# Performance work log

Hardware: AMD Instinct MI355X
Metric: run time of the kernel (lower is better)

## Reference

```python
import jax, jax.numpy as jnp
from jax import lax
import numpy as np

B, C, H, W = 16, 256, 96, 96
K = 11            # conv kernel size along one axis
C8 = C // 8       # query/key channels


def _conv(x, w, b):
    # 'same' conv in NCHW with OIHW weights; kernel is (kh,1) or (1,kw)
    kh, kw = w.shape[2], w.shape[3]
    y = lax.conv_general_dilated(
        x, w, window_strides=(1, 1),
        padding=((kh // 2, kh // 2), (kw // 2, kw // 2)),
        dimension_numbers=('NCHW', 'OIHW', 'NCHW'))
    return y + b[None, :, None, None]


def setup_inputs() -> dict:
    key = jax.random.key(0)
    ks = jax.random.split(key, 14)
    s = 0.05
    d = {
        'x':    jax.random.normal(ks[0], (B, C, H, W), jnp.float32),
        'wq_h': jax.random.normal(ks[1], (C8, C, K, 1), jnp.float32) * s,
        'bq_h': jax.random.normal(ks[2], (C8,), jnp.float32) * s,
        'wq_w': jax.random.normal(ks[3], (C8, C, 1, K), jnp.float32) * s,
        'bq_w': jax.random.normal(ks[4], (C8,), jnp.float32) * s,
        'wk_h': jax.random.normal(ks[5], (C8, C, K, 1), jnp.float32) * s,
        'bk_h': jax.random.normal(ks[6], (C8,), jnp.float32) * s,
        'wk_w': jax.random.normal(ks[7], (C8, C, 1, K), jnp.float32) * s,
        'bk_w': jax.random.normal(ks[8], (C8,), jnp.float32) * s,
        'wv_h': jax.random.normal(ks[9], (C, C, K, 1), jnp.float32) * s,
        'bv_h': jax.random.normal(ks[10], (C,), jnp.float32) * s,
        'wv_w': jax.random.normal(ks[11], (C, C, 1, K), jnp.float32) * s,
        'bv_w': jax.random.normal(ks[12], (C,), jnp.float32) * s,
        # gamma is a learned scalar (zero-init in torch); nonzero here so the
        # attention path contributes to the output
        'gamma': jax.random.normal(ks[13], (1,), jnp.float32) * 0.5,
    }
    return d


def reference(x, wq_h, bq_h, wq_w, bq_w, wk_h, bk_h, wk_w, bk_w,
              wv_h, bv_h, wv_w, bv_w, gamma):
    b, c, h, w = x.shape
    q_h = _conv(x, wq_h, bq_h)   # [B, C8, H, W]
    q_w = _conv(x, wq_w, bq_w)
    k_h = _conv(x, wk_h, bk_h)
    k_w = _conv(x, wk_w, bk_w)
    v_h = _conv(x, wv_h, bv_h)   # [B, C, H, W]
    v_w = _conv(x, wv_w, bv_w)
    # column (H-axis) attention energies: [B, H, W, H'] with -inf on h==h'
    e_h = jnp.einsum('bchw,bcHw->bhwH', q_h, k_h)
    diag = jnp.eye(h, dtype=bool)[None, :, None, :]  # [1, H, 1, H']
    e_h = jnp.where(diag, -jnp.inf, e_h)
    # row (W-axis) attention energies: [B, H, W, W']
    e_w = jnp.einsum('bchw,bchW->bhwW', q_w, k_w)
    # joint softmax over concatenated H'+W' axis
    att = jax.nn.softmax(jnp.concatenate([e_h, e_w], axis=-1), axis=-1)
    a_h = att[..., :h]           # [B, H, W, H']
    a_w = att[..., h:]           # [B, H, W, W']
    out_h = jnp.einsum('bcHw,bhwH->bchw', v_h, a_h)
    out_w = jnp.einsum('bchW,bhwW->bchw', v_w, a_w)
    return gamma * (out_h + out_w) + x
```

## Files before the change

kernel.cpp:

```cpp
#include <hip/hip_runtime.h>

constexpr int Bn = 16, Cn = 256, Hn = 96, Wn = 96, Pn = Hn * Wn;

#define DI static __device__ __forceinline__

struct alignas(16) U4 { unsigned a, b, c, d; };

typedef _Float16 f16x8 __attribute__((ext_vector_type(8)));
typedef float f32x4 __attribute__((ext_vector_type(4)));

#define GLOAD16(g, l) __builtin_amdgcn_global_load_lds( \
    (const __attribute__((address_space(1))) void*)(g), \
    (__attribute__((address_space(3))) void*)(l), 16, 0, 0)

__global__ void k_wt16(const float* __restrict__ w, _Float16* __restrict__ wt,
                       int co_n, int co_off, int co_tot) {
    int idx = blockIdx.x * 256 + threadIdx.x;
    if (idx >= co_n * 2816) return;
    int co = idx / 2816;
    int r  = idx - co * 2816;
    int c  = r / 11, t = r - c * 11;
    wt[((size_t)t * co_tot + co_off + co) * 256 + c] = (_Float16)w[idx];
}

__global__ __launch_bounds__(256) void k_xsplit(const float* __restrict__ x,
                                                _Float16* __restrict__ xh, _Float16* __restrict__ xl,
                                                _Float16* __restrict__ xhT, _Float16* __restrict__ xlT) {
    int b = blockIdx.y;
    int tid = threadIdx.x;
    int p = blockIdx.x * 128 + (tid >> 1);
    int half = tid & 1;
    int h = p / 96, w = p - h * 96;
    int pT = w * 96 + h;
    const float* xb = x + (size_t)b * Cn * Pn + p;
    size_t ob  = ((size_t)b * Pn + p) * 256;
    size_t obT = ((size_t)b * Pn + pT) * 256;
    for (int it = 0; it < 16; ++it) {
        int c0 = it * 16 + half * 8;
        f16x8 vh_, vl_;
#pragma unroll
        for (int i = 0; i < 8; ++i) {
            float f = xb[(size_t)(c0 + i) * Pn];
            _Float16 hh = (_Float16)f;
            vh_[i] = hh;
            vl_[i] = (_Float16)(f - (float)hh);
        }
        *(f16x8*)(xh + ob + c0) = vh_;
        *(f16x8*)(xl + ob + c0) = vl_;
        *(f16x8*)(xhT + obT + c0) = vh_;
        *(f16x8*)(xlT + obT + c0) = vl_;
    }
}

__global__ __launch_bounds__(256, 3) void k_conv_v(const _Float16* __restrict__ X0,
                                                   const _Float16* __restrict__ W0,
                                                   const float* __restrict__ b0a,
                                                   _Float16* __restrict__ o0,
                                                   const _Float16* __restrict__ X1,
                                                   const _Float16* __restrict__ W1,
                                                   const float* __restrict__ b1a,
                                                   _Float16* __restrict__ o1) {
    __shared__ char sm_raw[28672];
    const int tid = threadIdx.x;
    const int lane = tid & 63, wave = tid >> 6;
    const int wm = wave >> 1, wn = wave & 1;
    const int l15 = lane & 15, kg = lane >> 4;
    const int bx = blockIdx.x, co0 = blockIdx.y * 64;
    const int fam = blockIdx.z >> 4, b = blockIdx.z & 15;
    const _Float16* X  = fam ? X1 : X0;
    const _Float16* WT = fam ? W1 : W0;
    const float* bias  = fam ? b1a : b0a;
    _Float16* out      = fam ? o1 : o0;

    for (int z = tid; z < 1024; z += 256) {
        int bufo = (z >> 9) * 14336;
        int s = (z >> 7) & 3, off = z & 127;
        int Rbase = (s >> 1) * 112 + ((s & 1) ? 104 : 0);
        *(unsigned*)(sm_raw + bufo + Rbase * 64 + off * 4) = 0u;
    }

    f32x4 acc[2][6];
#pragma unroll
    for (int mf = 0; mf < 2; ++mf) {
        const float* bp = bias + co0 + wm * 32 + mf * 16 + kg * 4;
        f32x4 bv = { bp[0], bp[1], bp[2], bp[3] };
#pragma unroll
        for (int nf = 0; nf < 6; ++nf) acc[mf][nf] = bv;
    }

    const _Float16* Xb = X + ((size_t)b * Pn + bx * 192) * 256;
    const _Float16* Wb = WT + (size_t)(co0 + wm * 32 + l15) * 256 + kg * 8;

    auto STAGE = [&](int c0, int bufo) {
        for (int i = wave; i < 12; i += 4) {
            int rr = i / 6, wch = i - rr * 6;
            int row_local = 8 + wch * 16 + (lane >> 2);
            int kchunk = (lane & 3) ^ ((row_local >> 1) & 3);
            const _Float16* src = Xb + ((size_t)(rr * 96 + row_local - 8)) * 256 + c0 + kchunk * 8;
            char* dst = sm_raw + bufo + (rr * 112 + 8 + wch * 16) * 64;
            GLOAD16(src, dst);
        }
    };
    auto LDA = [&](f16x8* slot, const _Float16* tp) {
#pragma unroll
        for (int mf = 0; mf < 2; ++mf) slot[mf] = *(const f16x8*)(tp + mf * 4096);
    };
    auto LDB = [&](f16x8* dst, const char* Bb, int T) {
        int rl0 = 3 + l15 + T;
        const char* bp = Bb + (wn * 112 + rl0) * 64 + ((kg ^ ((rl0 >> 1) & 3)) << 4);
#pragma unroll
        for (int nf = 0; nf < 6; ++nf) dst[nf] = *(const f16x8*)(bp + nf * 1024);
    };

    STAGE(0, 0);
    __syncthreads();

    int cur = 0;
    for (int s8 = 0; s8 < 8; ++s8) {
        const int c0 = s8 * 32;
        const _Float16* wc = Wb + c0;
        f16x8 afc[2], afn[2];
        LDA(afc, wc);
        if (s8 < 7) STAGE(c0 + 32, (cur ^ 1) * 14336);
        const char* Bb = sm_raw + cur * 14336;
        f16x8 b0f[6], b1f[6];
        LDB(b0f, Bb, 0);
#pragma unroll
        for (int t = 0; t < 11; ++t) {
            if (t < 10) {
                LDA(afn, wc + (t + 1) * 65536);
                LDB((t & 1) ? b0f : b1f, Bb, t + 1);
            }
            const f16x8* bf = (t & 1) ? b1f : b0f;
            __builtin_amdgcn_s_setprio(1);
#pragma unroll
            for (int mf = 0; mf < 2; ++mf)
#pragma unroll
                for (int nf = 0; nf < 6; ++nf)
                    acc[mf][nf] = __builtin_amdgcn_mfma_f32_16x16x32_f16(afc[mf], bf[nf], acc[mf][nf], 0, 0, 0);
            __builtin_amdgcn_s_setprio(0);
            if (t < 10) {
#pragma unroll
                for (int mf = 0; mf < 2; ++mf) afc[mf] = afn[mf];
            }
        }
        __syncthreads();
        cur ^= 1;
    }

    _Float16* sb = (_Float16*)sm_raw;
#pragma unroll
    for (int mf = 0; mf < 2; ++mf)
#pragma unroll
        for (int nf = 0; nf < 6; ++nf)
#pragma unroll
            for (int r = 0; r < 4; ++r) {
                int row = wm * 32 + mf * 16 + kg * 4 + r;
                int p = wn * 96 + nf * 16 + l15;
                sb[row * 192 + p] = (_Float16)acc[mf][nf][r];
            }
    __syncthreads();
    for (int k = 0; k < 6; ++k) {
        int ci = tid + k * 256;
        int row = ci / 24, ch = ci - row * 24;
        U4 v = *(const U4*)(sm_raw + row * 384 + ch * 16);
        *(U4*)(out + ((size_t)b * 256 + co0 + row) * Pn + bx * 192 + ch * 8) = v;
    }
}

__global__ __launch_bounds__(256, 2) void k_conv_qk(const _Float16* __restrict__ Xh0,
                                                    const _Float16* __restrict__ Xl0,
                                                    const _Float16* __restrict__ W0,
                                                    const float* __restrict__ bq0, const float* __restrict__ bk0,
                                                    _Float16* __restrict__ q0, _Float16* __restrict__ k0,
                                                    const _Float16* __restrict__ Xh1,
                                                    const _Float16* __restrict__ Xl1,
                                                    const _Float16* __restrict__ W1,
                                                    const float* __restrict__ bq1, const float* __restrict__ bk1,
                                                    _Float16* __restrict__ q1, _Float16* __restrict__ k1) {
    __shared__ char sm_raw[57344];
    const int tid = threadIdx.x;
    const int lane = tid & 63, wave = tid >> 6;
    const int wm = wave >> 1, wn = wave & 1;
    const int l15 = lane & 15, kg = lane >> 4;
    const int bx = blockIdx.x;
    const int fam = blockIdx.z >> 4, b = blockIdx.z & 15;
    const _Float16* Xh = fam ? Xh1 : Xh0;
    const _Float16* Xl = fam ? Xl1 : Xl0;
    const _Float16* WT = fam ? W1 : W0;
    const float* bq = fam ? bq1 : bq0;
    const float* bk = fam ? bk1 : bk0;
    _Float16* q16 = fam ? q1 : q0;
    _Float16* k16 = fam ? k1 : k0;

    for (int z = tid; z < 2048; z += 256) {
        int bufo = (z >> 10) * 28672;
        int s = (z >> 7) & 7, off = z & 127;
        int Rbase = (s >> 1) * 112 + ((s & 1) ? 104 : 0);
        *(unsigned*)(sm_raw + bufo + Rbase * 64 + off * 4) = 0u;
    }

    f32x4 acc[2][6];
#pragma unroll
    for (int mf = 0; mf < 2; ++mf) {
        int cb = wm * 32 + mf * 16 + kg * 4;
        f32x4 bv;
#pragma unroll
        for (int r = 0; r < 4; ++r) {
            int co_l = cb + r;
            bv[r] = (co_l < 32) ? bq[co_l] : bk[co_l - 32];
        }
#pragma unroll
        for (int nf = 0; nf < 6; ++nf) acc[mf][nf] = bv;
    }

    const _Float16* Xbh = Xh + ((size_t)b * Pn + bx * 192) * 256;
    const _Float16* Xbl = Xl + ((size_t)b * Pn + bx * 192) * 256;
    const _Float16* Wb = WT + (size_t)(wm * 32 + l15) * 256 + kg * 8;

    auto STAGE = [&](int c0, int bufo) {
        for (int i = wave; i < 24; i += 4) {
            int a = i / 12, rr = (i / 6) & 1, wch = i % 6;
            int row_local = 8 + wch * 16 + (lane >> 2);
            int kchunk = (lane & 3) ^ ((row_local >> 1) & 3);
            const _Float16* base = (a == 0) ? Xbh : Xbl;
            const _Float16* src = base + ((size_t)(rr * 96 + row_local - 8)) * 256 + c0 + kchunk * 8;
            char* dst = sm_raw + bufo + ((a * 2 + rr) * 112 + 8 + wch * 16) * 64;
            GLOAD16(src, dst);
        }
    };
    auto LDBHL = [&](f16x8* dh, f16x8* dl, const char* Bb, int T) {
        int rl0 = 3 + l15 + T;
        const char* bp = Bb + (wn * 112 + rl0) * 64 + ((kg ^ ((rl0 >> 1) & 3)) << 4);
#pragma unroll
        for (int nf = 0; nf < 6; ++nf) {
            dh[nf] = *(const f16x8*)(bp + nf * 1024);
            dl[nf] = *(const f16x8*)(bp + 14336 + nf * 1024);
        }
    };

    STAGE(0, 0);
    __syncthreads();

    int cur = 0;
    for (int s8 = 0; s8 < 8; ++s8) {
        const int c0 = s8 * 32;
        const _Float16* wc = Wb + c0;
        f16x8 afc[2], afn[2];
#pragma unroll
        for (int mf = 0; mf < 2; ++mf) afc[mf] = *(const f16x8*)(wc + mf * 4096);
        if (s8 < 7) STAGE(c0 + 32, (cur ^ 1) * 28672);
        const char* Bb = sm_raw + cur * 28672;
#pragma unroll
        for (int t = 0; t < 11; ++t) {
            if (t < 10) {
#pragma unroll
                for (int mf = 0; mf < 2; ++mf)
                    afn[mf] = *(const f16x8*)(wc + (t + 1) * 16384 + mf * 4096);
            }
            f16x8 bh[6], bl[6];
            LDBHL(bh, bl, Bb, t);
            __builtin_amdgcn_s_setprio(1);
#pragma unroll
            for (int mf = 0; mf < 2; ++mf)
#pragma unroll
                for (int nf = 0; nf < 6; ++nf) {
                    acc[mf][nf] = __builtin_amdgcn_mfma_f32_16x16x32_f16(afc[mf], bh[nf], acc[mf][nf], 0, 0, 0);
                    acc[mf][nf] = __builtin_amdgcn_mfma_f32_16x16x32_f16(afc[mf], bl[nf], acc[mf][nf], 0, 0, 0);
                }
            __builtin_amdgcn_s_setprio(0);
            if (t < 10) {
#pragma unroll
                for (int mf = 0; mf < 2; ++mf) afc[mf] = afn[mf];
            }
        }
        __syncthreads();
        cur ^= 1;
    }

    __syncthreads();
    _Float16* sq = (_Float16*)sm_raw;
    _Float16* sk = (_Float16*)(sm_raw + 12288);
#pragma unroll
    for (int mf = 0; mf < 2; ++mf) {
        int cb = wm * 32 + mf * 16 + kg * 4;
#pragma unroll
        for (int r = 0; r < 4; ++r) {
            int co_l = cb + r;
            _Float16* arr = (co_l < 32) ? sq : sk;
            int c = co_l & 31;
#pragma unroll
            for (int nf = 0; nf < 6; ++nf) {
                int p = wn * 96 + nf * 16 + l15;
                arr[p * 32 + c] = (_Float16)acc[mf][nf][r];
            }
        }
    }
    __syncthreads();
    for (int j = 0; j < 6; ++j) {
        int idx = tid + j * 256;
        int mtx = idx >= 768;
        int e = idx - mtx * 768;
        int p = e >> 2, cg2 = e & 3;
        U4 v = *(const U4*)(sm_raw + mtx * 12288 + p * 64 + cg2 * 16);
        _Float16* dstb = mtx ? k16 : q16;
        *(U4*)(dstb + ((size_t)b * Pn + bx * 192 + p) * 32 + cg2 * 8) = v;
    }
}

DI void stage_qk16(const _Float16* qg, const _Float16* kg, char* Lq, char* Lk, int tid) {
    for (int i = tid; i < 768; i += 256) {
        int mtx = i >= 384;
        int e = i - mtx * 384;
        int p = e >> 2, ch = e & 3;
        const _Float16* src = (mtx ? kg : qg) + p * 32 + ch * 8;
        f16x8 v = *(const f16x8*)src;
        char* dst = (mtx ? Lk : Lq) + p * 64 + ((ch ^ ((p >> 1) & 3)) << 4);
        *(f16x8*)dst = v;
    }
}

DI void mfma_e(const char* Lq, const char* Lk, float* Ef, int lane, int wave) {
    int l15 = lane & 15, kg = lane >> 4;
    int wm = wave >> 1, wn = wave & 1;
    f16x8 qa[3], kb[3];
#pragma unroll
    for (int i = 0; i < 3; ++i) {
        int pr = wm * 48 + i * 16 + l15;
        qa[i] = *(const f16x8*)(Lq + pr * 64 + ((kg ^ ((pr >> 1) & 3)) << 4));
        int pc = wn * 48 + i * 16 + l15;
        kb[i] = *(const f16x8*)(Lk + pc * 64 + ((kg ^ ((pc >> 1) & 3)) << 4));
    }
#pragma unroll
    for (int i = 0; i < 3; ++i)
#pragma unroll
        for (int j = 0; j < 3; ++j) {
            f32x4 a = { 0.f, 0.f, 0.f, 0.f };
            a = __builtin_amdgcn_mfma_f32_16x16x32_f16(qa[i], kb[j], a, 0, 0, 0);
#pragma unroll
            for (int r = 0; r < 4; ++r) {
                int row = wm * 48 + i * 16 + kg * 4 + r;
                int col = wn * 48 + j * 16 + l15;
                Ef[row * 97 + col] = a[r];
            }
        }
}

__global__ __launch_bounds__(256) void k_p1(const _Float16* __restrict__ q16, const _Float16* __restrict__ k16,
                                            float* __restrict__ mh, float* __restrict__ lh) {
    __shared__ char L[49536];
    float* Ef = (float*)L;
    char* Lq = L + 37248;
    char* Lk = L + 43392;
    const int tid = threadIdx.x, lane = tid & 63, wave = tid >> 6;
    const int w = blockIdx.x, b = blockIdx.y;
    const _Float16* qg = q16 + ((size_t)b * Pn + w * 96) * 32;
    const _Float16* kg = k16 + ((size_t)b * Pn + w * 96) * 32;
    stage_qk16(qg, kg, Lq, Lk, tid);
    __syncthreads();
    mfma_e(Lq, Lk, Ef, lane, wave);
    __syncthreads();
    if (tid < 96) {
        int h = tid;
        const float* er = Ef + h * 97;
        float m = -INFINITY;
        for (int j = 0; j < 96; ++j) if (j != h) m = fmaxf(m, er[j]);
        float l = 0.f;
        for (int j = 0; j < 96; ++j) if (j != h) l += __expf(er[j] - m);
        mh[((size_t)b * 96 + w) * 96 + h] = m;
        lh[((size_t)b * 96 + w) * 96 + h] = l;
    }
}

__global__ __launch_bounds__(256) void k_p2(const _Float16* __restrict__ q16, const _Float16* __restrict__ k16,
                                            const _Float16* __restrict__ V,
                                            const float* __restrict__ mh, const float* __restrict__ lh,
                                            float* __restrict__ mo, float* __restrict__ lo,
                                            _Float16* __restrict__ outw) {
    __shared__ char L[56448];
    float* Ef = (float*)L;
    char* LA  = L + 37248;
    char* Lq  = L + 37248;
    char* Lk  = L + 43392;
    float* Marr = (float*)(L + 55680);
    float* Linv = (float*)(L + 56064);
    const int tid = threadIdx.x, lane = tid & 63, wave = tid >> 6;
    const int l15 = lane & 15, kg = lane >> 4;
    const int h = blockIdx.x, b = blockIdx.y;
    const _Float16* qg = q16 + ((size_t)b * Pn + h * 96) * 32;
    const _Float16* kgp = k16 + ((size_t)b * Pn + h * 96) * 32;
    stage_qk16(qg, kgp, Lq, Lk, tid);
    __syncthreads();
    mfma_e(Lq, Lk, Ef, lane, wave);
    __syncthreads();
    if (tid < 96) {
        int wq = tid;
        const float* er = Ef + wq * 97;
        float mw = -INFINITY;
        for (int j = 0; j < 96; ++j) mw = fmaxf(mw, er[j]);
        float lw = 0.f;
        for (int j = 0; j < 96; ++j) lw += __expf(er[j] - mw);
        float mhv = mh[((size_t)b * 96 + wq) * 96 + h];
        float lhv = lh[((size_t)b * 96 + wq) * 96 + h];
        float m = fmaxf(mhv, mw);
        float l = lhv * __expf(mhv - m) + lw * __expf(mw - m);
        mo[((size_t)b * 96 + h) * 96 + wq] = m;
        lo[((size_t)b * 96 + h) * 96 + wq] = l;
        Marr[wq] = m;
        Linv[wq] = 1.f / l;
    }
    __syncthreads();
    if (tid < 192) {
        int r = tid >> 1, half = tid & 1;
        float m = Marr[r], li = Linv[r];
        const float* er = Ef + r * 97;
        for (int cc = 0; cc < 6; ++cc) {
            int chunk = half * 6 + cc;
            f16x8 av;
#pragma unroll
            for (int jj = 0; jj < 8; ++jj)
                av[jj] = (_Float16)(__expf(er[chunk * 8 + jj] - m) * li);
            *(f16x8*)(LA + r * 192 + ((chunk ^ ((r >> 1) & 3)) << 4)) = av;
        }
    }
    __syncthreads();
    f32x4 acc[4][6];
#pragma unroll
    for (int mf = 0; mf < 4; ++mf)
#pragma unroll
        for (int nf = 0; nf < 6; ++nf) acc[mf][nf] = f32x4{ 0.f, 0.f, 0.f, 0.f };
    const _Float16* vb = V + ((size_t)b * 256 + wave * 64 + l15) * Pn + h * 96 + kg * 8;
    f16x8 va[4][3];
#pragma unroll
    for (int mf = 0; mf < 4; ++mf)
#pragma unroll
        for (int ks = 0; ks < 3; ++ks)
            va[mf][ks] = *(const f16x8*)(vb + (size_t)mf * 16 * Pn + ks * 32);
#pragma unroll
    for (int ks = 0; ks < 3; ++ks)
#pragma unroll
        for (int nf = 0; nf < 6; ++nf) {
            int wq = nf * 16 + l15;
            int chunk = ks * 4 + kg;
            f16x8 bv = *(const f16x8*)(LA + wq * 192 + ((chunk ^ ((wq >> 1) & 3)) << 4));
#pragma unroll
            for (int mf = 0; mf < 4; ++mf)
                acc[mf][nf] = __builtin_amdgcn_mfma_f32_16x16x32_f16(va[mf][ks], bv, acc[mf][nf], 0, 0, 0);
        }
    _Float16* ob = outw + ((size_t)b * 256) * Pn + h * 96;
#pragma unroll
    for (int mf = 0; mf < 4; ++mf)
#pragma unroll
        for (int nf = 0; nf < 6; ++nf)
#pragma unroll
            for (int r = 0; r < 4; ++r) {
                int c = wave * 64 + mf * 16 + kg * 4 + r;
                ob[(size_t)c * Pn + nf * 16 + l15] = (_Float16)acc[mf][nf][r];
            }
}

__global__ __launch_bounds__(256) void k_p3(const _Float16* __restrict__ q16, const _Float16* __restrict__ k16,
                                            const _Float16* __restrict__ V,
                                            const float* __restrict__ mo, const float* __restrict__ lo,
                                            _Float16* __restrict__ pT) {
    __shared__ char L[56448];
    float* Ef = (float*)L;
    char* LA  = L + 37248;
    char* Lq  = L + 37248;
    char* Lk  = L + 43392;
    float* Marr = (float*)(L + 55680);
    float* Linv = (float*)(L + 56064);
    const int tid = threadIdx.x, lane = tid & 63, wave = tid >> 6;
    const int l15 = lane & 15, kg = lane >> 4;
    const int w = blockIdx.x, b = blockIdx.y;
    const _Float16* qg = q16 + ((size_t)b * Pn + w * 96) * 32;
    const _Float16* kgp = k16 + ((size_t)b * Pn + w * 96) * 32;
    stage_qk16(qg, kgp, Lq, Lk, tid);
    __syncthreads();
    mfma_e(Lq, Lk, Ef, lane, wave);
    __syncthreads();
    if (tid < 96) {
        int hq = tid;
        Marr[hq] = mo[((size_t)b * 96 + hq) * 96 + w];
        Linv[hq] = 1.f / lo[((size_t)b * 96 + hq) * 96 + w];
    }
    __syncthreads();
    if (tid < 192) {
        int r = tid >> 1, half = tid & 1;
        float m = Marr[r], li = Linv[r];
        const float* er = Ef + r * 97;
        for (int cc = 0; cc < 6; ++cc) {
            int chunk = half * 6 + cc;
            f16x8 av;
#pragma unroll
            for (int jj = 0; jj < 8; ++jj) {
                int col = chunk * 8 + jj;
                av[jj] = (col == r) ? (_Float16)0.f
                                    : (_Float16)(__expf(er[col] - m) * li);
            }
            *(f16x8*)(LA + r * 192 + ((chunk ^ ((r >> 1) & 3)) << 4)) = av;
        }
    }
    __syncthreads();
    f32x4 acc[4][6];
#pragma unroll
    for (int mf = 0; mf < 4; ++mf)
#pragma unroll
        for (int nf = 0; nf < 6; ++nf) acc[mf][nf] = f32x4{ 0.f, 0.f, 0.f, 0.f };
    const _Float16* vb = V + ((size_t)b * 256 + wave * 64 + l15) * Pn + w * 96 + kg * 8;
    f16x8 va[4][3];
#pragma unroll
    for (int mf = 0; mf < 4; ++mf)
#pragma unroll
        for (int ks = 0; ks < 3; ++ks)
            va[mf][ks] = *(const f16x8*)(vb + (size_t)mf * 16 * Pn + ks * 32);
#pragma unroll
    for (int ks = 0; ks < 3; ++ks)
#pragma unroll
        for (int nf = 0; nf < 6; ++nf) {
            int hq = nf * 16 + l15;
            int chunk = ks * 4 + kg;
            f16x8 bv = *(const f16x8*)(LA + hq * 192 + ((chunk ^ ((hq >> 1) & 3)) << 4));
#pragma unroll
            for (int mf = 0; mf < 4; ++mf)
                acc[mf][nf] = __builtin_amdgcn_mfma_f32_16x16x32_f16(va[mf][ks], bv, acc[mf][nf], 0, 0, 0);
        }
    _Float16* pb = pT + ((size_t)b * 256) * Pn + w * 96;
#pragma unroll
    for (int mf = 0; mf < 4; ++mf)
#pragma unroll
        for (int nf = 0; nf < 6; ++nf)
#pragma unroll
            for (int r = 0; r < 4; ++r) {
                int c = wave * 64 + mf * 16 + kg * 4 + r;
                pb[(size_t)c * Pn + nf * 16 + l15] = (_Float16)acc[mf][nf][r];
            }
}

__global__ __launch_bounds__(256) void k_combine(const _Float16* __restrict__ pT,
                                                 const _Float16* __restrict__ ow,
                                                 const float* __restrict__ x,
                                                 const float* __restrict__ gamma,
                                                 float* __restrict__ out) {
    __shared__ float T[32][33];
    int bh = blockIdx.x, bw = blockIdx.y;
    size_t ib = (size_t)blockIdx.z * Pn;
    int tx = threadIdx.x, ty = threadIdx.y;
#pragma unroll
    for (int i = 0; i < 4; ++i) {
        int r = bw * 32 + ty + i * 8;
        T[ty + i * 8][tx] = (float)pT[ib + (size_t)r * 96 + bh * 32 + tx];
    }
    __syncthreads();
    float g = gamma[0];
#pragma unroll
    for (int i = 0; i < 4; ++i) {
        int hh = bh * 32 + ty + i * 8, ww = bw * 32 + tx;
        size_t o = ib + (size_t)hh * 96 + ww;
        out[o] = g * (T[tx][ty + i * 8] + (float)ow[o]) + x[o];
    }
}

extern "C" void kernel_launch(void* const* d_in, const int* in_sizes, int n_in,
                              void* d_out, int out_size, void* d_ws, size_t ws_size,
                              hipStream_t stream) {
    (void)in_sizes; (void)n_in; (void)out_size; (void)ws_size;
    const float* x   = (const float*)d_in[0];
    const float* wqh = (const float*)d_in[1];
    const float* bqh = (const float*)d_in[2];
    const float* wqw = (const float*)d_in[3];
    const float* bqw = (const float*)d_in[4];
    const float* wkh = (const float*)d_in[5];
    const float* bkh = (const float*)d_in[6];
    const float* wkw = (const float*)d_in[7];
    const float* bkw = (const float*)d_in[8];
    const float* wvh = (const float*)d_in[9];
    const float* bvh = (const float*)d_in[10];
    const float* wvw = (const float*)d_in[11];
    const float* bvw = (const float*)d_in[12];
    const float* gam = (const float*)d_in[13];
    float* out = (float*)d_out;

    char* ws = (char*)d_ws;
    size_t off = 0;
    auto alloc = [&](size_t bytes) -> char* {
        char* p = ws + off;
        off = (off + bytes + 255) & ~(size_t)255;
        return p;
    };
    const size_t IMG = (size_t)Bn * Cn * Pn;
    const size_t QK16 = (size_t)Bn * Pn * 32;

    _Float16* xh  = (_Float16*)alloc(IMG * 2);
    _Float16* xl  = (_Float16*)alloc(IMG * 2);
    _Float16* xhT = (_Float16*)alloc(IMG * 2);
    _Float16* xlT = (_Float16*)alloc(IMG * 2);
    _Float16* qh16 = (_Float16*)alloc(QK16 * 2);
    _Float16* kh16 = (_Float16*)alloc(QK16 * 2);
    _Float16* qw16 = (_Float16*)alloc(QK16 * 2);
    _Float16* kw16 = (_Float16*)alloc(QK16 * 2);
    float* mh = (float*)alloc((size_t)Bn * Pn * 4);
    float* lh = (float*)alloc((size_t)Bn * Pn * 4);
    float* mo = (float*)alloc((size_t)Bn * Pn * 4);
    float* lo = (float*)alloc((size_t)Bn * Pn * 4);
    _Float16* wqkh  = (_Float16*)alloc((size_t)11 * 64 * 256 * 2);
    _Float16* wqkw  = (_Float16*)alloc((size_t)11 * 64 * 256 * 2);
    _Float16* wvh16 = (_Float16*)alloc((size_t)11 * 256 * 256 * 2);
    _Float16* wvw16 = (_Float16*)alloc((size_t)11 * 256 * 256 * 2);
    _Float16* vh = xlT;
    _Float16* vw = xl;
    _Float16* pT = xhT;
    _Float16* ow16 = xh;

    const int gq = (32 * 2816 + 255) / 256;
    const int gv = (256 * 2816 + 255) / 256;
    k_wt16<<<gq, 256, 0, stream>>>(wqh, wqkh, 32, 0, 64);
    k_wt16<<<gq, 256, 0, stream>>>(wkh, wqkh, 32, 32, 64);
    k_wt16<<<gq, 256, 0, stream>>>(wqw, wqkw, 32, 0, 64);
    k_wt16<<<gq, 256, 0, stream>>>(wkw, wqkw, 32, 32, 64);
    k_wt16<<<gv, 256, 0, stream>>>(wvh, wvh16, 256, 0, 256);
    k_wt16<<<gv, 256, 0, stream>>>(wvw, wvw16, 256, 0, 256);

    k_xsplit<<<dim3(72, 16), 256, 0, stream>>>(x, xh, xl, xhT, xlT);

    k_conv_qk<<<dim3(48, 1, 32), 256, 0, stream>>>(xhT, xlT, wqkh, bqh, bkh, qh16, kh16,
                                                   xh,  xl,  wqkw, bqw, bkw, qw16, kw16);
    k_conv_v <<<dim3(48, 4, 32), 256, 0, stream>>>(xhT, wvh16, bvh, vh,
                                                   xh,  wvw16, bvw, vw);

    k_p1<<<dim3(96, 16), 256, 0, stream>>>(qh16, kh16, mh, lh);
    k_p2<<<dim3(96, 16), 256, 0, stream>>>(qw16, kw16, vw, mh, lh, mo, lo, ow16);
    k_p3<<<dim3(96, 16), 256, 0, stream>>>(qh16, kh16, vh, mo, lo, pT);

    k_combine<<<dim3(3, 3, Bn * Cn), dim3(32, 8), 0, stream>>>(pT, ow16, x, gam, out);
}
```

Baseline: 1.163 ms.

## Double conv_v pixel tile per block and add XCD-aware block swizzle

The value-conv kernel now computes 384 pixels per block instead of 192, using 24 accumulator tiles per wave and doubled LDS staging, so each weight fragment loaded is reused across twice as many MFMAs. The B-operand double-buffering across taps is removed in favour of loading all 12 fragments per tap. Both conv kernels also remap block indices with a modulo-8 swizzle so neighbouring work lands on the same XCD for cache locality. The cost is more registers and LDS, which lowers occupancy to 2 blocks/CU, and less latency hiding for the LDS loads.

Result: faster. 988.5 us (-15.0%).

```diff
diff --git a/kernel.cpp b/kernel.cpp
--- a/kernel.cpp
+++ b/kernel.cpp
@@ -52,7 +52,7 @@
     }
 }
 
-__global__ __launch_bounds__(256, 3) void k_conv_v(const _Float16* __restrict__ X0,
+__global__ __launch_bounds__(256, 2) void k_conv_v(const _Float16* __restrict__ X0,
                                                    const _Float16* __restrict__ W0,
                                                    const float* __restrict__ b0a,
                                                    _Float16* __restrict__ o0,
@@ -60,44 +60,49 @@
                                                    const _Float16* __restrict__ W1,
                                                    const float* __restrict__ b1a,
                                                    _Float16* __restrict__ o1) {
-    __shared__ char sm_raw[28672];
+    __shared__ char sm_raw[57344];
     const int tid = threadIdx.x;
     const int lane = tid & 63, wave = tid >> 6;
     const int wm = wave >> 1, wn = wave & 1;
     const int l15 = lane & 15, kg = lane >> 4;
-    const int bx = blockIdx.x, co0 = blockIdx.y * 64;
-    const int fam = blockIdx.z >> 4, b = blockIdx.z & 15;
+    int fid = blockIdx.x + 24 * (blockIdx.y + 4 * blockIdx.z);
+    int swz = (fid & 7) * 384 + (fid >> 3);
+    const int bx = swz % 24;
+    int rest = swz / 24;
+    const int co0 = (rest & 3) * 64;
+    const int z = rest >> 2;
+    const int fam = z >> 4, b = z & 15;
     const _Float16* X  = fam ? X1 : X0;
     const _Float16* WT = fam ? W1 : W0;
     const float* bias  = fam ? b1a : b0a;
     _Float16* out      = fam ? o1 : o0;
 
-    for (int z = tid; z < 1024; z += 256) {
-        int bufo = (z >> 9) * 14336;
-        int s = (z >> 7) & 3, off = z & 127;
+    for (int zz = tid; zz < 2048; zz += 256) {
+        int bufo = (zz >> 10) * 28672;
+        int s = (zz >> 7) & 7, off = zz & 127;
         int Rbase = (s >> 1) * 112 + ((s & 1) ? 104 : 0);
         *(unsigned*)(sm_raw + bufo + Rbase * 64 + off * 4) = 0u;
     }
 
-    f32x4 acc[2][6];
+    f32x4 acc[2][12];
 #pragma unroll
     for (int mf = 0; mf < 2; ++mf) {
         const float* bp = bias + co0 + wm * 32 + mf * 16 + kg * 4;
         f32x4 bv = { bp[0], bp[1], bp[2], bp[3] };
 #pragma unroll
-        for (int nf = 0; nf < 6; ++nf) acc[mf][nf] = bv;
-    }
-
-    const _Float16* Xb = X + ((size_t)b * Pn + bx * 192) * 256;
+        for (int j = 0; j < 12; ++j) acc[mf][j] = bv;
+    }
+
+    const _Float16* Xb = X + ((size_t)b * Pn + bx * 384) * 256;
     const _Float16* Wb = WT + (size_t)(co0 + wm * 32 + l15) * 256 + kg * 8;
 
     auto STAGE = [&](int c0, int bufo) {
-        for (int i = wave; i < 12; i += 4) {
-            int rr = i / 6, wch = i - rr * 6;
+        for (int i = wave; i < 24; i += 4) {
+            int s = i / 6, wch = i - s * 6;
             int row_local = 8 + wch * 16 + (lane >> 2);
             int kchunk = (lane & 3) ^ ((row_local >> 1) & 3);
-            const _Float16* src = Xb + ((size_t)(rr * 96 + row_local - 8)) * 256 + c0 + kchunk * 8;
-            char* dst = sm_raw + bufo + (rr * 112 + 8 + wch * 16) * 64;
+            const _Float16* src = Xb + ((size_t)(s * 96 + row_local - 8)) * 256 + c0 + kchunk * 8;
+            char* dst = sm_raw + bufo + (s * 112 + 8 + wch * 16) * 64;
             GLOAD16(src, dst);
         }
     };
@@ -107,9 +112,12 @@
     };
     auto LDB = [&](f16x8* dst, const char* Bb, int T) {
         int rl0 = 3 + l15 + T;
-        const char* bp = Bb + (wn * 112 + rl0) * 64 + ((kg ^ ((rl0 >> 1) & 3)) << 4);
-#pragma unroll
-        for (int nf = 0; nf < 6; ++nf) dst[nf] = *(const f16x8*)(bp + nf * 1024);
+        const char* bp = Bb + (wn * 224 + rl0) * 64 + ((kg ^ ((rl0 >> 1) & 3)) << 4);
+#pragma unroll
+        for (int s = 0; s < 2; ++s)
+#pragma unroll
+            for (int nf = 0; nf < 6; ++nf)
+                dst[s * 6 + nf] = *(const f16x8*)(bp + s * 7168 + nf * 1024);
     };
 
     STAGE(0, 0);
@@ -121,23 +129,19 @@
         const _Float16* wc = Wb + c0;
         f16x8 afc[2], afn[2];
         LDA(afc, wc);
-        if (s8 < 7) STAGE(c0 + 32, (cur ^ 1) * 14336);
-        const char* Bb = sm_raw + cur * 14336;
-        f16x8 b0f[6], b1f[6];
-        LDB(b0f, Bb, 0);
+        if (s8 < 7) STAGE(c0 + 32, (cur ^ 1) * 28672);
+        const char* Bb = sm_raw + cur * 28672;
+        f16x8 bf[12];
 #pragma unroll
         for (int t = 0; t < 11; ++t) {
-            if (t < 10) {
-                LDA(afn, wc + (t + 1) * 65536);
-                LDB((t & 1) ? b0f : b1f, Bb, t + 1);
-            }
-            const f16x8* bf = (t & 1) ? b1f : b0f;
+            if (t < 10) LDA(afn, wc + (t + 1) * 65536);
+            LDB(bf, Bb, t);
             __builtin_amdgcn_s_setprio(1);
 #pragma unroll
             for (int mf = 0; mf < 2; ++mf)
 #pragma unroll
-                for (int nf = 0; nf < 6; ++nf)
-                    acc[mf][nf] = __builtin_amdgcn_mfma_f32_16x16x32_f16(afc[mf], bf[nf], acc[mf][nf], 0, 0, 0);
+                for (int j = 0; j < 12; ++j)
+                    acc[mf][j] = __builtin_amdgcn_mfma_f32_16x16x32_f16(afc[mf], bf[j], acc[mf][j], 0, 0, 0);
             __builtin_amdgcn_s_setprio(0);
             if (t < 10) {
 #pragma unroll
@@ -152,19 +156,19 @@
 #pragma unroll
     for (int mf = 0; mf < 2; ++mf)
 #pragma unroll
-        for (int nf = 0; nf < 6; ++nf)
+        for (int j = 0; j < 12; ++j)
 #pragma unroll
             for (int r = 0; r < 4; ++r) {
                 int row = wm * 32 + mf * 16 + kg * 4 + r;
-                int p = wn * 96 + nf * 16 + l15;
-                sb[row * 192 + p] = (_Float16)acc[mf][nf][r];
-            }
-    __syncthreads();
-    for (int k = 0; k < 6; ++k) {
+                int p = wn * 192 + (j / 6) * 96 + (j % 6) * 16 + l15;
+                sb[row * 384 + p] = (_Float16)acc[mf][j][r];
+            }
+    __syncthreads();
+    for (int k = 0; k < 12; ++k) {
         int ci = tid + k * 256;
-        int row = ci / 24, ch = ci - row * 24;
-        U4 v = *(const U4*)(sm_raw + row * 384 + ch * 16);
-        *(U4*)(out + ((size_t)b * 256 + co0 + row) * Pn + bx * 192 + ch * 8) = v;
+        int row = ci / 48, ch = ci - row * 48;
+        U4 v = *(const U4*)(sm_raw + row * 768 + ch * 16);
+        *(U4*)(out + ((size_t)b * 256 + co0 + row) * Pn + bx * 384 + ch * 8) = v;
     }
 }
 
@@ -183,8 +187,11 @@
     const int lane = tid & 63, wave = tid >> 6;
     const int wm = wave >> 1, wn = wave & 1;
     const int l15 = lane & 15, kg = lane >> 4;
-    const int bx = blockIdx.x;
-    const int fam = blockIdx.z >> 4, b = blockIdx.z & 15;
+    int fid = blockIdx.x + 48 * blockIdx.z;
+    int swz = (fid & 7) * 192 + (fid >> 3);
+    const int bx = swz % 48;
+    const int zz0 = swz / 48;
+    const int fam = zz0 >> 4, b = zz0 & 15;
     const _Float16* Xh = fam ? Xh1 : Xh0;
     const _Float16* Xl = fam ? Xl1 : Xl0;
     const _Float16* WT = fam ? W1 : W0;
@@ -625,7 +632,7 @@
 
     k_conv_qk<<<dim3(48, 1, 32), 256, 0, stream>>>(xhT, xlT, wqkh, bqh, bkh, qh16, kh16,
                                                    xh,  xl,  wqkw, bqw, bkw, qw16, kw16);
-    k_conv_v <<<dim3(48, 4, 32), 256, 0, stream>>>(xhT, wvh16, bvh, vh,
+    k_conv_v <<<dim3(24, 4, 32), 256, 0, stream>>>(xhT, wvh16, bvh, vh,
                                                    xh,  wvw16, bvw, vw);
 
     k_p1<<<dim3(96, 16), 256, 0, stream>>>(qh16, kh16, mh, lh);
```
